# Optimization experiments

Measured on AMD Instinct MI355X. Metric: run time of the kernel, lower is better.

The kernel has to match this reference:

```python
import jax, jax.numpy as jnp
import numpy as np

H = W = 32      # latent grid
WS = 8          # window size
NH = 8          # heads
C = 512         # channels
SHIFTS = (0, WS // 2)  # depth-2 Swin stage: W-MSA then SW-MSA


def _rel_pos_index(ws):
    coords = np.stack(np.meshgrid(np.arange(ws), np.arange(ws), indexing='ij'))
    flat = coords.reshape(2, -1)
    rel = (flat[:, :, None] - flat[:, None, :]).transpose(1, 2, 0).copy()
    rel[:, :, 0] += ws - 1
    rel[:, :, 1] += ws - 1
    rel[:, :, 0] *= 2 * ws - 1
    return jnp.asarray(rel.sum(-1))  # (ws*ws, ws*ws) int


def _attn_mask(h, w, ws, shift):
    img = np.zeros((h, w))
    cnt = 0
    sl = (slice(0, -ws), slice(-ws, -shift), slice(-shift, None))
    for hs in sl:
        for wsl in sl:
            img[hs, wsl] = cnt
            cnt += 1
    mw = img.reshape(h // ws, ws, w // ws, ws).transpose(0, 2, 1, 3).reshape(-1, ws * ws)
    m = mw[:, None, :] - mw[:, :, None]  # matches unsqueeze(1) - unsqueeze(2)
    return jnp.asarray(np.where(m != 0, -100.0, 0.0).astype(np.float32))  # (nW, N, N)


def _ln(x, g, b, eps=1e-5):
    mu = x.mean(-1, keepdims=True)
    var = ((x - mu) ** 2).mean(-1, keepdims=True)
    return (x - mu) * jax.lax.rsqrt(var + eps) * g + b


def _swin_block(x, shift, mask, rpi, n1g, n1b, qw, qb, rpb, pw, pb, n2g, n2b, f1w, f1b, f2w, f2b):
    B, L, Cc = x.shape
    N = WS * WS
    hd = Cc // NH
    shortcut = x
    h = _ln(x, n1g, n1b).reshape(B, H, W, Cc)
    if shift > 0:
        h = jnp.roll(h, (-shift, -shift), (1, 2))
    # window partition -> (B*nW, N, C)
    hw = h.reshape(B, H // WS, WS, W // WS, WS, Cc).transpose(0, 1, 3, 2, 4, 5).reshape(-1, N, Cc)
    qkv = (hw @ qw + qb).reshape(-1, N, 3, NH, hd).transpose(2, 0, 3, 1, 4)
    q, k, v = qkv[0], qkv[1], qkv[2]
    attn = jnp.einsum('bhnd,bhmd->bhnm', q * (hd ** -0.5), k)
    bias = rpb[rpi.reshape(-1)].reshape(N, N, NH).transpose(2, 0, 1)  # (NH, N, N)
    attn = attn + bias[None]
    if mask is not None:
        nW = mask.shape[0]
        attn = attn.reshape(-1, nW, NH, N, N) + mask[None, :, None]
        attn = attn.reshape(-1, NH, N, N)
    attn = jax.nn.softmax(attn, axis=-1)
    o = jnp.einsum('bhnm,bhmd->bhnd', attn, v).transpose(0, 2, 1, 3).reshape(-1, N, Cc)
    o = o @ pw + pb
    # window reverse
    o = o.reshape(B, H // WS, W // WS, WS, WS, Cc).transpose(0, 1, 3, 2, 4, 5).reshape(B, H, W, Cc)
    if shift > 0:
        o = jnp.roll(o, (shift, shift), (1, 2))
    x = shortcut + o.reshape(B, L, Cc)
    h2 = _ln(x, n2g, n2b)
    x = x + (jax.nn.gelu(h2 @ f1w + f1b, approximate=False) @ f2w + f2b)
    return x


def setup_inputs() -> dict:
    key = jax.random.key(0)
    ks = jax.random.split(key, 8)
    B, D, K = 32, 2, 4096
    s = 0.02
    return {
        'x': jax.random.normal(ks[0], (B, H * W, C), jnp.float32),
        'norm1_g': jnp.ones((D, C), jnp.float32),
        'norm1_b': jnp.zeros((D, C), jnp.float32),
        'qkv_w': jax.random.normal(ks[1], (D, C, 3 * C), jnp.float32) * s,
        'qkv_b': jnp.zeros((D, 3 * C), jnp.float32),
        'rpb_table': jax.random.normal(ks[2], (D, (2 * WS - 1) ** 2, NH), jnp.float32) * s,
        'proj_w': jax.random.normal(ks[3], (D, C, C), jnp.float32) * s,
        'proj_b': jnp.zeros((D, C), jnp.float32),
        'norm2_g': jnp.ones((D, C), jnp.float32),
        'norm2_b': jnp.zeros((D, C), jnp.float32),
        'fc1_w': jax.random.normal(ks[4], (D, C, 4 * C), jnp.float32) * s,
        'fc1_b': jnp.zeros((D, 4 * C), jnp.float32),
        'fc2_w': jax.random.normal(ks[5], (D, 4 * C, C), jnp.float32) * s,
        'fc2_b': jnp.zeros((D, C), jnp.float32),
        'codebook': jax.random.normal(ks[6], (K, C), jnp.float32),
    }


def reference(x, norm1_g, norm1_b, qkv_w, qkv_b, rpb_table, proj_w, proj_b,
              norm2_g, norm2_b, fc1_w, fc1_b, fc2_w, fc2_b, codebook):
    B, L, Cc = x.shape
    rpi = _rel_pos_index(WS)
    masks = [None, _attn_mask(H, W, WS, SHIFTS[1])]
    for i, shift in enumerate(SHIFTS):
        x = _swin_block(x, shift, masks[i], rpi,
                        norm1_g[i], norm1_b[i], qkv_w[i], qkv_b[i], rpb_table[i],
                        proj_w[i], proj_b[i], norm2_g[i], norm2_b[i],
                        fc1_w[i], fc1_b[i], fc2_w[i], fc2_b[i])
    # nearest-neighbor codebook quantization (cdist + argmin + gather)
    flat = x.reshape(-1, Cc)
    d = ((flat ** 2).sum(-1, keepdims=True)
         - 2.0 * flat @ codebook.T
         + (codebook ** 2).sum(-1))  # (B*L, K)
    idx = jnp.argmin(d, axis=-1)
    quant = codebook[idx]
    # straight-through estimator
    quant = flat + jax.lax.stop_gradient(quant - flat)
    return quant.reshape(B, L, Cc), idx.reshape(B, L)
```

## Files before the change

### kernel.cpp

```cpp
#include <hip/hip_runtime.h>
#include <math.h>

#define DEV __device__ __forceinline__

typedef __attribute__((ext_vector_type(8))) _Float16 f16x8;
typedef __attribute__((ext_vector_type(8))) short short8;
typedef __attribute__((ext_vector_type(4))) float f32x4;

namespace {

constexpr int C = 512;
constexpr int ROWS = 32768;
constexpr float LSCALE = 2048.0f;
constexpr float LINV   = 1.0f / 2048.0f;
constexpr float F16MIN = 6.1035156e-5f;

DEV void f2hsplit(float x, short& hs, short& ls) {
  _Float16 h = (_Float16)x;
  float hf = (float)h;
  if (fabsf(hf) < F16MIN) { h = (_Float16)0.0f; hf = 0.f; }
  _Float16 l = (_Float16)((x - hf) * LSCALE);
  if (fabsf((float)l) < F16MIN) l = (_Float16)0.0f;
  hs = __builtin_bit_cast(short, h);
  ls = __builtin_bit_cast(short, l);
}

DEV unsigned umn(unsigned a, unsigned b) { return a < b ? a : b; }
DEV unsigned umx(unsigned a, unsigned b) { return a > b ? a : b; }

DEV unsigned packkey(float d, int col) {
  unsigned u = __builtin_bit_cast(unsigned, d);
  u = (u & 0x80000000u) ? ~u : (u | 0x80000000u);
  return (u & 0xFFFFF000u) | (unsigned)col;
}
DEV float unpackd(unsigned k) {
  unsigned u = (k & 0x80000000u) ? (k ^ 0x80000000u) : ~k;
  return __builtin_bit_cast(float, u);
}

DEV int rowmap(int r, int shift) {
  int b  = r >> 10;
  int w  = (r >> 6) & 15;
  int wy = w >> 2, wx = w & 3;
  int ii = r & 63;
  int iy = ii >> 3, ix = ii & 7;
  int y = (wy * 8 + iy + shift) & 31;
  int x = (wx * 8 + ix + shift) & 31;
  return (b << 10) + (y << 5) + x;
}

DEV int region(int y) { return (y < 24) ? 0 : ((y < 28) ? 1 : 2); }

typedef __attribute__((address_space(1))) const unsigned int gu32;
typedef __attribute__((address_space(3))) unsigned int lu32;
DEV void gload16(const void* g, void* l) {
  __builtin_amdgcn_global_load_lds((gu32*)g, (lu32*)l, 16, 0, 0);
}

DEV void tilemap(int Mt, int Nt, int GM, int& mt, int& nt) {
  int bid = blockIdx.y * Mt + blockIdx.x;
  if ((Mt & 7) == 0) {
    int xcd = bid & 7, idx = bid >> 3;
    int Mt8 = Mt >> 3;
    if (GM > Mt8) GM = Mt8;
    int span = GM * Nt;
    int g = idx / span, rem = idx % span;
    nt = rem / GM;
    mt = xcd * Mt8 + g * GM + rem % GM;
  } else {
    mt = blockIdx.x; nt = blockIdx.y;
  }
}

__global__ __launch_bounds__(256) void ln_split_kernel(
    const float* __restrict__ src, short* __restrict__ Hp, short* __restrict__ Lp,
    const float* __restrict__ g, const float* __restrict__ b,
    int shift, int windowed) {
  int wid  = (blockIdx.x * 256 + threadIdx.x) >> 6;
  int lane = threadIdx.x & 63;
  if (wid >= ROWS) return;
  int srcRow = windowed ? rowmap(wid, shift) : wid;
  const float* s = src + (size_t)srcRow * C + lane * 8;
  float v[8];
  *(float4*)(v)     = *(const float4*)(s);
  *(float4*)(v + 4) = *(const float4*)(s + 4);
  float sum = 0.f;
#pragma unroll
  for (int j = 0; j < 8; j++) sum += v[j];
#pragma unroll
  for (int o = 32; o >= 1; o >>= 1) sum += __shfl_xor(sum, o);
  float mu = sum * (1.0f / 512.0f);
  float vs = 0.f;
#pragma unroll
  for (int j = 0; j < 8; j++) { float d = v[j] - mu; vs += d * d; }
#pragma unroll
  for (int o = 32; o >= 1; o >>= 1) vs += __shfl_xor(vs, o);
  float rs = rsqrtf(vs * (1.0f / 512.0f) + 1e-5f);
  float gg[8], bb[8];
  *(float4*)gg       = *(const float4*)&g[lane * 8];
  *(float4*)(gg + 4) = *(const float4*)&g[lane * 8 + 4];
  *(float4*)bb       = *(const float4*)&b[lane * 8];
  *(float4*)(bb + 4) = *(const float4*)&b[lane * 8 + 4];
  short8 hv, lv;
#pragma unroll
  for (int j = 0; j < 8; j++) {
    float o8 = (v[j] - mu) * rs * gg[j] + bb[j];
    short hh, ll;
    f2hsplit(o8, hh, ll);
    hv[j] = hh; lv[j] = ll;
  }
  *(short8*)&Hp[(size_t)wid * C + lane * 8] = hv;
  *(short8*)&Lp[(size_t)wid * C + lane * 8] = lv;
}

__global__ __launch_bounds__(256) void rowss_kernel(
    const float* __restrict__ src, float* __restrict__ dst, int nrows) {
  int wid  = (blockIdx.x * 256 + threadIdx.x) >> 6;
  int lane = threadIdx.x & 63;
  if (wid >= nrows) return;
  const float* s = src + (size_t)wid * C + lane * 8;
  float4 a  = *(const float4*)s;
  float4 b4 = *(const float4*)(s + 4);
  float sum = a.x*a.x + a.y*a.y + a.z*a.z + a.w*a.w
            + b4.x*b4.x + b4.y*b4.y + b4.z*b4.z + b4.w*b4.w;
#pragma unroll
  for (int o = 32; o >= 1; o >>= 1) sum += __shfl_xor(sum, o);
  if (lane == 0) dst[wid] = sum;
}

__global__ __launch_bounds__(256) void wconvT_kernel(
    const float* __restrict__ W, short* __restrict__ Hp, short* __restrict__ Lp,
    int K, int N) {
  __shared__ float t[32][33];
  int tx = threadIdx.x, ty = threadIdx.y;
  int n0 = blockIdx.x * 32, k0 = blockIdx.y * 32;
#pragma unroll
  for (int r = 0; r < 4; r++) {
    int k = ty + r * 8;
    t[k][tx] = W[(size_t)(k0 + k) * N + n0 + tx];
  }
  __syncthreads();
#pragma unroll
  for (int r = 0; r < 4; r++) {
    int n = ty + r * 8;
    short h, l;
    f2hsplit(t[tx][n], h, l);
    Hp[(size_t)(n0 + n) * K + k0 + tx] = h;
    Lp[(size_t)(n0 + n) * K + k0 + tx] = l;
  }
}

__global__ __launch_bounds__(256) void wconv_kernel(
    const float* __restrict__ W, short* __restrict__ Hp, short* __restrict__ Lp) {
  size_t i = ((size_t)blockIdx.x * 256 + threadIdx.x) * 4;
  float4 a = *(const float4*)&W[i];
  float v[4] = {a.x, a.y, a.z, a.w};
  short hv[4], lv[4];
#pragma unroll
  for (int j = 0; j < 4; j++) f2hsplit(v[j], hv[j], lv[j]);
  *(short4*)&Hp[i] = *(short4*)hv;
  *(short4*)&Lp[i] = *(short4*)lv;
}

template <int EPI>
__global__ __launch_bounds__(512) void mgemm(
    const short* __restrict__ Ah, const short* __restrict__ Al,
    const short* __restrict__ Bh, const short* __restrict__ Bl,
    const int K, const float* __restrict__ bias,
    float* __restrict__ outF, short* __restrict__ outH, short* __restrict__ outL,
    const int ldo,
    const float* __restrict__ resid, const int rowOff, const int perm, const int shift) {
  __shared__ short lds[32768];
  int mt, nt;
  tilemap(gridDim.x, gridDim.y, 4, mt, nt);
  const int m0 = mt * 128, n0 = nt * 128;
  const int t  = threadIdx.x;
  const int wv = t >> 6, ln = t & 63;
  const int wr = (wv >> 2) * 64, wc = (wv & 3) * 32;
  const int l15 = ln & 15, l4 = ln >> 4;

  f32x4 accH[4][2], accL[4][2];
#pragma unroll
  for (int mf = 0; mf < 4; mf++)
#pragma unroll
    for (int nf = 0; nf < 2; nf++) {
      accH[mf][nf] = (f32x4){0.f, 0.f, 0.f, 0.f};
      accL[mf][nf] = (f32x4){0.f, 0.f, 0.f, 0.f};
    }

  const int srow = ln >> 2;
  const int scol = ((ln & 3) ^ ((ln >> 3) & 3)) * 8;

  auto stage = [&](int buf, int k0) {
    short* b = lds + buf * 16384;
    size_t ra = (size_t)(m0 + wv * 16 + srow) * K + k0 + scol;
    size_t rb = (size_t)(n0 + wv * 16 + srow) * K + k0 + scol;
    gload16(Ah + ra, b + wv * 512);
    gload16(Bh + rb, b + 4096 + wv * 512);
    gload16(Al + ra, b + 8192 + wv * 512);
    gload16(Bl + rb, b + 12288 + wv * 512);
  };
  auto frag = [&](const short* lt, int rbase) -> f16x8 {
    int r = rbase + l15;
    int kc = l4 ^ ((r >> 1) & 3);
    return *(const f16x8*)(lt + (r >> 4) * 512 + (r & 15) * 32 + kc * 8);
  };

  stage(0, 0);
  __syncthreads();
  int cur = 0;
  for (int k0 = 0; k0 < K; k0 += 32) {
    if (k0 + 32 < K) stage(cur ^ 1, k0 + 32);
    const short* base = lds + cur * 16384;
    f16x8 ah[4], bh[2], bl[2];
#pragma unroll
    for (int mf = 0; mf < 4; mf++) ah[mf] = frag(base, wr + mf * 16);
#pragma unroll
    for (int nf = 0; nf < 2; nf++) bh[nf] = frag(base + 4096, wc + nf * 16);
    __builtin_amdgcn_s_setprio(1);
#pragma unroll
    for (int mf = 0; mf < 4; mf++)
#pragma unroll
      for (int nf = 0; nf < 2; nf++)
        accH[mf][nf] = __builtin_amdgcn_mfma_f32_16x16x32_f16(ah[mf], bh[nf], accH[mf][nf], 0, 0, 0);
    __builtin_amdgcn_s_setprio(0);
#pragma unroll
    for (int nf = 0; nf < 2; nf++) bl[nf] = frag(base + 12288, wc + nf * 16);
    __builtin_amdgcn_s_setprio(1);
#pragma unroll
    for (int mf = 0; mf < 4; mf++)
#pragma unroll
      for (int nf = 0; nf < 2; nf++)
        accL[mf][nf] = __builtin_amdgcn_mfma_f32_16x16x32_f16(ah[mf], bl[nf], accL[mf][nf], 0, 0, 0);
#pragma unroll
    for (int mf = 0; mf < 4; mf++) {
      f16x8 al = frag(base + 8192, wr + mf * 16);
#pragma unroll
      for (int nf = 0; nf < 2; nf++)
        accL[mf][nf] = __builtin_amdgcn_mfma_f32_16x16x32_f16(al, bh[nf], accL[mf][nf], 0, 0, 0);
    }
    __builtin_amdgcn_s_setprio(0);
    __syncthreads();
    cur ^= 1;
  }

  f32x4 acc[4][2];
#pragma unroll
  for (int mf = 0; mf < 4; mf++)
#pragma unroll
    for (int nf = 0; nf < 2; nf++)
#pragma unroll
      for (int r = 0; r < 4; r++)
        acc[mf][nf][r] = fmaf(accL[mf][nf][r], LINV, accH[mf][nf][r]);

  if (EPI == 0) {
#pragma unroll
    for (int mf = 0; mf < 4; mf++)
#pragma unroll
      for (int r = 0; r < 4; r++) {
        int row = m0 + wr + mf * 16 + l4 * 4 + r;
        float* op = outF + (size_t)row * ldo;
#pragma unroll
        for (int nf = 0; nf < 2; nf++) {
          int col = n0 + wc + nf * 16 + l15;
          op[col] = acc[mf][nf][r] + bias[col];
        }
      }
  } else if (EPI == 1) {
#pragma unroll
    for (int mf = 0; mf < 4; mf++)
#pragma unroll
      for (int r = 0; r < 4; r++) {
        int row = m0 + wr + mf * 16 + l4 * 4 + r;
#pragma unroll
        for (int nf = 0; nf < 2; nf++) {
          int col = n0 + wc + nf * 16 + l15;
          float v = acc[mf][nf][r] + bias[col];
          v = 0.5f * v * (1.0f + erff(v * 0.70710678118654752f));
          short h, l;
          f2hsplit(v, h, l);
          outH[(size_t)row * ldo + col] = h;
          outL[(size_t)row * ldo + col] = l;
        }
      }
  } else {
#pragma unroll
    for (int mf = 0; mf < 4; mf++)
#pragma unroll
      for (int r = 0; r < 4; r++) {
        int row = m0 + wr + mf * 16 + l4 * 4 + r;
        int orow = perm ? rowmap(row, shift) : (row + rowOff);
        const float* rp = resid + (size_t)orow * ldo;
        float* op = outF + (size_t)orow * ldo;
#pragma unroll
        for (int nf = 0; nf < 2; nf++) {
          int col = n0 + wc + nf * 16 + l15;
          float v = rp[col] + acc[mf][nf][r] + bias[col];
          op[col] = v;
          if (EPI == 4) {
            short h, l;
            f2hsplit(v, h, l);
            outH[(size_t)orow * ldo + col] = h;
            outL[(size_t)orow * ldo + col] = l;
          }
        }
      }
  }
}

__global__ __launch_bounds__(512) void vqgemm(
    const short* __restrict__ Ah, const short* __restrict__ Bh,
    const float* __restrict__ c2, unsigned* __restrict__ pk) {
  __shared__ short lds[12288];
  const int bid = blockIdx.x;
  const int xcd = bid & 7, idx = bid >> 3;
  const int g  = idx >> 7;
  const int ny = (idx >> 3) & 15;
  const int mi = idx & 7;
  const int m0 = (xcd * 32 + g * 8 + mi) * 128;
  const int n0 = ny * 256;
  const int K = 512;
  const int t  = threadIdx.x;
  const int wv = t >> 6, ln = t & 63;
  const int wr = (wv >> 2) * 64, wc = (wv & 3) * 64;
  const int l15 = ln & 15, l4 = ln >> 4;

  f32x4 acc[4][4];
#pragma unroll
  for (int mf = 0; mf < 4; mf++)
#pragma unroll
    for (int nf = 0; nf < 4; nf++) acc[mf][nf] = (f32x4){0.f, 0.f, 0.f, 0.f};

  const int srow = ln >> 2;
  const int scol = ((ln & 3) ^ ((ln >> 3) & 3)) * 8;

  short* As = lds;
  short* Bs = lds + 4096;

  auto frag = [&](const short* lt, int rbase) -> f16x8 {
    int r = rbase + l15;
    int kc = l4 ^ ((r >> 1) & 3);
    return *(const f16x8*)(lt + (r >> 4) * 512 + (r & 15) * 32 + kc * 8);
  };

  for (int k0 = 0; k0 < K; k0 += 32) {
#pragma unroll
    for (int q = 0; q < 3; q++) {
      int s = wv * 3 + q;
      int isA = (s < 8);
      int c = isA ? s : (s - 8);
      const short* src = isA ? Ah : Bh;
      short* dst = (isA ? As : Bs) + c * 512;
      int rowbase = (isA ? m0 : n0) + c * 16;
      size_t ga = (size_t)(rowbase + srow) * K + k0 + scol;
      gload16(src + ga, dst);
    }
    __syncthreads();
    f16x8 ah[4], bh[4];
#pragma unroll
    for (int mf = 0; mf < 4; mf++) ah[mf] = frag(As, wr + mf * 16);
#pragma unroll
    for (int nf = 0; nf < 4; nf++) bh[nf] = frag(Bs, wc + nf * 16);
    __builtin_amdgcn_s_setprio(1);
#pragma unroll
    for (int mf = 0; mf < 4; mf++)
#pragma unroll
      for (int nf = 0; nf < 4; nf++)
        acc[mf][nf] = __builtin_amdgcn_mfma_f32_16x16x32_f16(ah[mf], bh[nf], acc[mf][nf], 0, 0, 0);
    __builtin_amdgcn_s_setprio(0);
    __syncthreads();
  }

  unsigned* hk = (unsigned*)(void*)lds;
#pragma unroll
  for (int mf = 0; mf < 4; mf++)
#pragma unroll
    for (int r = 0; r < 4; r++) {
      int wrow = wr + mf * 16 + l4 * 4 + r;
      unsigned k1 = 0xFFFFFFFFu, k2 = 0xFFFFFFFFu;
#pragma unroll
      for (int nf = 0; nf < 4; nf++) {
        int col = n0 + wc + nf * 16 + l15;
        float d = c2[col] - 2.0f * acc[mf][nf][r];
        unsigned kk = packkey(d, col);
        if (kk < k1) { k2 = k1; k1 = kk; }
        else if (kk < k2) { k2 = kk; }
      }
#pragma unroll
      for (int o = 1; o <= 8; o <<= 1) {
        unsigned b1 = (unsigned)__shfl_xor((int)k1, o);
        unsigned b2 = (unsigned)__shfl_xor((int)k2, o);
        unsigned m1 = umn(k1, b1);
        unsigned m2 = umn(umx(k1, b1), umn(k2, b2));
        k1 = m1; k2 = m2;
      }
      if (l15 == 0) {
        hk[wrow * 8 + (wv & 3) * 2 + 0] = k1;
        hk[wrow * 8 + (wv & 3) * 2 + 1] = k2;
      }
    }
  __syncthreads();
  if (t < 128) {
    unsigned q1[4], q2[4];
#pragma unroll
    for (int i = 0; i < 4; i++) {
      q1[i] = hk[t * 8 + i * 2];
      q2[i] = hk[t * 8 + i * 2 + 1];
    }
    unsigned a1 = umn(q1[0], q1[1]);
    unsigned a2 = umn(umx(q1[0], q1[1]), umn(q2[0], q2[1]));
    unsigned b1 = umn(q1[2], q1[3]);
    unsigned b2 = umn(umx(q1[2], q1[3]), umn(q2[2], q2[3]));
    unsigned m1 = umn(a1, b1);
    unsigned m2 = umn(umx(a1, b1), umn(a2, b2));
    size_t base = (size_t)(m0 + t) * 32 + ny * 2;
    pk[base + 0] = m1;
    pk[base + 1] = m2;
  }
}

__global__ __launch_bounds__(256) void vq_out_kernel(
    const unsigned* __restrict__ pk, const float* __restrict__ x,
    const float* __restrict__ cb,
    float* __restrict__ outq, float* __restrict__ outidx) {
  int r = blockIdx.x * 4 + (threadIdx.x >> 6);
  int lane = threadIdx.x & 63;
  unsigned key = (lane < 32) ? pk[(size_t)r * 32 + lane] : 0xFFFFFFFFu;
  unsigned kmin = key;
#pragma unroll
  for (int o = 32; o >= 1; o >>= 1) kmin = umn(kmin, (unsigned)__shfl_xor((int)kmin, o));
  float dmin = unpackd(kmin);
  unsigned long long mask = __ballot(lane < 32 && unpackd(key) <= dmin + 2.0f);

  const float* xr = x + (size_t)r * C + lane * 8;
  float4 xa = *(const float4*)xr;
  float4 xb = *(const float4*)(xr + 4);

  float bestd = 3.4e38f;
  int   besti = 0x7fffffff;
  while (mask) {
    int l = __ffsll(mask) - 1;
    mask &= mask - 1;
    int col = ((unsigned)__shfl((int)key, l)) & 0xFFFu;
    const float* cr = cb + (size_t)col * C + lane * 8;
    float4 ca = *(const float4*)cr;
    float4 cb4 = *(const float4*)(cr + 4);
    float s = 0.f;
    s = fmaf(ca.x, ca.x - 2.f * xa.x, s);
    s = fmaf(ca.y, ca.y - 2.f * xa.y, s);
    s = fmaf(ca.z, ca.z - 2.f * xa.z, s);
    s = fmaf(ca.w, ca.w - 2.f * xa.w, s);
    s = fmaf(cb4.x, cb4.x - 2.f * xb.x, s);
    s = fmaf(cb4.y, cb4.y - 2.f * xb.y, s);
    s = fmaf(cb4.z, cb4.z - 2.f * xb.z, s);
    s = fmaf(cb4.w, cb4.w - 2.f * xb.w, s);
#pragma unroll
    for (int o = 32; o >= 1; o >>= 1) s += __shfl_xor(s, o);
    if (s < bestd || (s == bestd && col < besti)) { bestd = s; besti = col; }
  }
  const float4* src = (const float4*)(cb + (size_t)besti * C + lane * 8);
  float4*       dst = (float4*)(outq + (size_t)r * C + lane * 8);
  dst[0] = src[0];
  dst[1] = src[1];
  if (lane == 0) outidx[r] = (float)besti;
}

__global__ __launch_bounds__(256) void attn_kernel(
    const float* __restrict__ qkv,
    const float* __restrict__ rpb,
    short* __restrict__ Hout, short* __restrict__ Lout,
    int winOff, int shift) {
  int wl = blockIdx.x;
  int h  = blockIdx.y;
  int t  = threadIdx.x;
  __shared__ float q[64][64], k[64][64], v[64][64];
  float (*pT)[64] = q;

  const float* base = qkv + (size_t)wl * 64 * 1536 + h * 64;
#pragma unroll
  for (int rep = 0; rep < 4; rep++) {
    int f = t + rep * 256;
    int i = f >> 4, dq = (f & 15) * 4;
    const float* rowp = base + (size_t)i * 1536 + dq;
    float4 qv = *(const float4*)(rowp);
    float4 kv = *(const float4*)(rowp + 512);
    float4 vv = *(const float4*)(rowp + 1024);
    q[i][dq] = qv.x * 0.125f; q[i][dq + 1] = qv.y * 0.125f;
    q[i][dq + 2] = qv.z * 0.125f; q[i][dq + 3] = qv.w * 0.125f;
    *(float4*)&k[i][dq] = kv;
    *(float4*)&v[i][dq] = vv;
  }
  __syncthreads();

  int i  = t >> 2;
  int jg = t & 3;
  int wim = (winOff + wl) & 15;
  int wy = wim >> 2, wx = wim & 3;
  int iy = i >> 3, ix = i & 7;

  float qreg[64];
#pragma unroll
  for (int d = 0; d < 64; d += 4) *(float4*)&qreg[d] = *(float4*)&q[i][d];
  __syncthreads();

  int ci = 0;
  if (shift) ci = region(wy * 8 + iy) * 3 + region(wx * 8 + ix);

  float sc[16];
#pragma unroll
  for (int jj = 0; jj < 16; jj++) {
    int j = jg * 16 + jj;
    float s = 0.f;
#pragma unroll
    for (int d = 0; d < 64; d += 4) {
      float4 kv = *(float4*)&k[j][d];
      s = fmaf(qreg[d], kv.x, s);
      s = fmaf(qreg[d + 1], kv.y, s);
      s = fmaf(qreg[d + 2], kv.z, s);
      s = fmaf(qreg[d + 3], kv.w, s);
    }
    int jy = j >> 3, jx = j & 7;
    s += rpb[((iy - jy + 7) * 15 + (ix - jx + 7)) * 8 + h];
    if (shift) {
      int cj = region(wy * 8 + jy) * 3 + region(wx * 8 + jx);
      if (ci != cj) s -= 100.0f;
    }
    sc[jj] = s;
  }
  float mx = sc[0];
#pragma unroll
  for (int jj = 1; jj < 16; jj++) mx = fmaxf(mx, sc[jj]);
  mx = fmaxf(mx, __shfl_xor(mx, 1));
  mx = fmaxf(mx, __shfl_xor(mx, 2));
  float sum = 0.f;
#pragma unroll
  for (int jj = 0; jj < 16; jj++) { sc[jj] = expf(sc[jj] - mx); sum += sc[jj]; }
  sum += __shfl_xor(sum, 1);
  sum += __shfl_xor(sum, 2);
  float inv = 1.0f / sum;
#pragma unroll
  for (int jj = 0; jj < 16; jj++) pT[jg * 16 + jj][i] = sc[jj] * inv;
  __syncthreads();

  float accv[16];
#pragma unroll
  for (int dd = 0; dd < 16; dd++) accv[dd] = 0.f;
  for (int j = 0; j < 64; j++) {
    float pij = pT[j][i];
#pragma unroll
    for (int dd = 0; dd < 16; dd += 4) {
      float4 vv = *(float4*)&v[j][jg * 16 + dd];
      accv[dd]     = fmaf(pij, vv.x, accv[dd]);
      accv[dd + 1] = fmaf(pij, vv.y, accv[dd + 1]);
      accv[dd + 2] = fmaf(pij, vv.z, accv[dd + 2]);
      accv[dd + 3] = fmaf(pij, vv.w, accv[dd + 3]);
    }
  }
  size_t obase = ((size_t)(winOff + wl) * 64 + i) * 512 + h * 64 + jg * 16;
  short8 hv, lv;
#pragma unroll
  for (int half = 0; half < 2; half++) {
#pragma unroll
    for (int j = 0; j < 8; j++) {
      short hh, ll;
      f2hsplit(accv[half * 8 + j], hh, ll);
      hv[j] = hh; lv[j] = ll;
    }
    *(short8*)&Hout[obase + half * 8] = hv;
    *(short8*)&Lout[obase + half * 8] = lv;
  }
}

}

extern "C" void kernel_launch(void* const* d_in, const int* in_sizes, int n_in,
                              void* d_out, int out_size, void* d_ws, size_t ws_size,
                              hipStream_t stream) {
  const float* x_in = (const float*)d_in[0];
  const float* n1g  = (const float*)d_in[1];
  const float* n1b  = (const float*)d_in[2];
  const float* qkvw = (const float*)d_in[3];
  const float* qkvb = (const float*)d_in[4];
  const float* rpb  = (const float*)d_in[5];
  const float* pw   = (const float*)d_in[6];
  const float* pb   = (const float*)d_in[7];
  const float* n2g  = (const float*)d_in[8];
  const float* n2b  = (const float*)d_in[9];
  const float* f1w  = (const float*)d_in[10];
  const float* f1b  = (const float*)d_in[11];
  const float* f2w  = (const float*)d_in[12];
  const float* f2b_ = (const float*)d_in[13];
  const float* cb   = (const float*)d_in[14];

  float* outq   = (float*)d_out;
  float* outidx = outq + 16777216;
  short* Hbuf = (short*)d_out;
  short* Lbuf = Hbuf + (size_t)ROWS * 512;

  char* ws = (char*)d_ws;
  float* Abuf = (float*)ws;
  short* Wb   = (short*)(ws + ((size_t)64 << 20));
  char*  Cbuf = ws + ((size_t)96 << 20);
  const int Rrows = (ws_size >= ((size_t)232 << 20)) ? 16384
                  : (ws_size >= ((size_t)160 << 20)) ? 8192
                  : (ws_size >= ((size_t)128 << 20)) ? 4096 : 2048;

  const int SZ_QKV = 512 * 1536, SZ_P = 512 * 512, SZ_F1 = 512 * 2048, SZ_F2 = 2048 * 512;
  const int PB = (SZ_QKV + SZ_P + SZ_F1 + SZ_F2) * 2;
  short* cbH = Wb + (size_t)2 * PB;
  short* cbL = cbH + 4096 * 512;

  for (int blk = 0; blk < 2; blk++) {
    short* base = Wb + (size_t)blk * PB;
    short* qH = base;          short* qL = qH + SZ_QKV;
    short* pH = qL + SZ_QKV;   short* pL = pH + SZ_P;
    short* f1H = pL + SZ_P;    short* f1L = f1H + SZ_F1;
    short* f2H = f1L + SZ_F1;  short* f2L = f2H + SZ_F2;
    wconvT_kernel<<<dim3(48, 16), dim3(32, 8), 0, stream>>>(qkvw + (size_t)blk * SZ_QKV, qH, qL, 512, 1536);
    wconvT_kernel<<<dim3(16, 16), dim3(32, 8), 0, stream>>>(pw + (size_t)blk * SZ_P, pH, pL, 512, 512);
    wconvT_kernel<<<dim3(64, 16), dim3(32, 8), 0, stream>>>(f1w + (size_t)blk * SZ_F1, f1H, f1L, 512, 2048);
    wconvT_kernel<<<dim3(16, 64), dim3(32, 8), 0, stream>>>(f2w + (size_t)blk * SZ_F2, f2H, f2L, 2048, 512);
  }
  wconv_kernel<<<2048, 256, 0, stream>>>(cb, cbH, cbL);

  const int nch = ROWS / Rrows;
  for (int blk = 0; blk < 2; blk++) {
    short* base = Wb + (size_t)blk * PB;
    short* qH = base;          short* qL = qH + SZ_QKV;
    short* pH = qL + SZ_QKV;   short* pL = pH + SZ_P;
    short* f1H = pL + SZ_P;    short* f1L = f1H + SZ_F1;
    short* f2H = f1L + SZ_F1;  short* f2L = f2H + SZ_F2;
    const float* xcur = blk ? (const float*)Abuf : x_in;
    int shift = blk ? 4 : 0;

    ln_split_kernel<<<8192, 256, 0, stream>>>(xcur, Hbuf, Lbuf, n1g + blk * 512, n1b + blk * 512, shift, 1);

    float* Cq = (float*)Cbuf;
    for (int ch = 0; ch < nch; ch++) {
      int r0 = ch * Rrows;
      mgemm<0><<<dim3(Rrows / 128, 12), 512, 0, stream>>>(
          Hbuf + (size_t)r0 * 512, Lbuf + (size_t)r0 * 512, qH, qL, 512,
          qkvb + blk * 1536, Cq, nullptr, nullptr, 1536,
          nullptr, 0, 0, 0);
      attn_kernel<<<dim3(Rrows / 64, 8), 256, 0, stream>>>(
          Cq, rpb + blk * 1800, Hbuf, Lbuf, r0 >> 6, shift);
    }

    mgemm<2><<<dim3(256, 4), 512, 0, stream>>>(
        Hbuf, Lbuf, pH, pL, 512, pb + blk * 512,
        Abuf, nullptr, nullptr, 512,
        blk ? (const float*)Abuf : x_in, 0, 1, shift);

    ln_split_kernel<<<8192, 256, 0, stream>>>(Abuf, Hbuf, Lbuf, n2g + blk * 512, n2b + blk * 512, 0, 0);

    short* gh = (short*)Cbuf;
    short* gl = gh + (size_t)Rrows * 2048;
    for (int ch = 0; ch < nch; ch++) {
      int r0 = ch * Rrows;
      mgemm<1><<<dim3(Rrows / 128, 16), 512, 0, stream>>>(
          Hbuf + (size_t)r0 * 512, Lbuf + (size_t)r0 * 512, f1H, f1L, 512,
          f1b + blk * 2048, nullptr, gh, gl, 2048,
          nullptr, 0, 0, 0);
      if (blk == 0) {
        mgemm<2><<<dim3(Rrows / 128, 4), 512, 0, stream>>>(
            gh, gl, f2H, f2L, 2048, f2b_ + blk * 512,
            Abuf, nullptr, nullptr, 512,
            Abuf, r0, 0, 0);
      } else {
        mgemm<4><<<dim3(Rrows / 128, 4), 512, 0, stream>>>(
            gh, gl, f2H, f2L, 2048, f2b_ + blk * 512,
            Abuf, Hbuf, Lbuf, 512,
            Abuf, r0, 0, 0);
      }
    }
  }

  float*    c2  = (float*)Cbuf;
  unsigned* pkb = (unsigned*)(Cbuf + ((size_t)64 << 10));
  rowss_kernel<<<1024, 256, 0, stream>>>(cb, c2, 4096);
  vqgemm<<<4096, 512, 0, stream>>>(Hbuf, cbH, c2, pkb);
  vq_out_kernel<<<8192, 256, 0, stream>>>(pkb, Abuf, cb, outq, outidx);
}
```

Before: 2.237 ms.

## Retile attention kernel into 4x4 register blocks with padded shared memory

```diff
diff --git a/kernel.cpp b/kernel.cpp
--- a/kernel.cpp
+++ b/kernel.cpp
@@ -470,11 +470,13 @@
     const float* __restrict__ rpb,
     short* __restrict__ Hout, short* __restrict__ Lout,
     int winOff, int shift) {
+  constexpr int LDW = 68;
+  __shared__ float q[64 * LDW], k[64 * LDW], v[64 * LDW];
+  float* pT = q;
+
   int wl = blockIdx.x;
   int h  = blockIdx.y;
   int t  = threadIdx.x;
-  __shared__ float q[64][64], k[64][64], v[64][64];
-  float (*pT)[64] = q;
 
   const float* base = qkv + (size_t)wl * 64 * 1536 + h * 64;
 #pragma unroll
@@ -485,89 +487,116 @@
     float4 qv = *(const float4*)(rowp);
     float4 kv = *(const float4*)(rowp + 512);
     float4 vv = *(const float4*)(rowp + 1024);
-    q[i][dq] = qv.x * 0.125f; q[i][dq + 1] = qv.y * 0.125f;
-    q[i][dq + 2] = qv.z * 0.125f; q[i][dq + 3] = qv.w * 0.125f;
-    *(float4*)&k[i][dq] = kv;
-    *(float4*)&v[i][dq] = vv;
+    qv.x *= 0.125f; qv.y *= 0.125f; qv.z *= 0.125f; qv.w *= 0.125f;
+    *(float4*)&q[i * LDW + dq] = qv;
+    *(float4*)&k[i * LDW + dq] = kv;
+    *(float4*)&v[i * LDW + dq] = vv;
   }
   __syncthreads();
 
-  int i  = t >> 2;
-  int jg = t & 3;
-  int wim = (winOff + wl) & 15;
-  int wy = wim >> 2, wx = wim & 3;
-  int iy = i >> 3, ix = i & 7;
-
-  float qreg[64];
-#pragma unroll
-  for (int d = 0; d < 64; d += 4) *(float4*)&qreg[d] = *(float4*)&q[i][d];
+  const int rgrp = t >> 4, cgrp = t & 15;
+  const int wim = (winOff + wl) & 15;
+  const int wy = wim >> 2, wx = wim & 3;
+
+  float s[4][4];
+#pragma unroll
+  for (int r = 0; r < 4; r++)
+#pragma unroll
+    for (int c = 0; c < 4; c++) s[r][c] = 0.f;
+#pragma unroll
+  for (int dch = 0; dch < 16; dch++) {
+    float4 q4[4], k4[4];
+#pragma unroll
+    for (int r = 0; r < 4; r++) q4[r] = *(float4*)&q[(rgrp * 4 + r) * LDW + dch * 4];
+#pragma unroll
+    for (int c = 0; c < 4; c++) k4[c] = *(float4*)&k[(cgrp + 16 * c) * LDW + dch * 4];
+#pragma unroll
+    for (int r = 0; r < 4; r++)
+#pragma unroll
+      for (int c = 0; c < 4; c++) {
+        s[r][c] = fmaf(q4[r].x, k4[c].x, s[r][c]);
+        s[r][c] = fmaf(q4[r].y, k4[c].y, s[r][c]);
+        s[r][c] = fmaf(q4[r].z, k4[c].z, s[r][c]);
+        s[r][c] = fmaf(q4[r].w, k4[c].w, s[r][c]);
+      }
+  }
+#pragma unroll
+  for (int r = 0; r < 4; r++) {
+    int i = rgrp * 4 + r;
+    int iy = i >> 3, ix = i & 7;
+    int ci = shift ? (region(wy * 8 + iy) * 3 + region(wx * 8 + ix)) : 0;
+#pragma unroll
+    for (int c = 0; c < 4; c++) {
+      int j = cgrp + 16 * c;
+      int jy = j >> 3, jx = j & 7;
+      s[r][c] += rpb[((iy - jy + 7) * 15 + (ix - jx + 7)) * 8 + h];
+      if (shift) {
+        int cj = region(wy * 8 + jy) * 3 + region(wx * 8 + jx);
+        if (ci != cj) s[r][c] -= 100.0f;
+      }
+    }
+  }
+  float p[4][4];
+#pragma unroll
+  for (int r = 0; r < 4; r++) {
+    float mx = fmaxf(fmaxf(s[r][0], s[r][1]), fmaxf(s[r][2], s[r][3]));
+#pragma unroll
+    for (int o = 1; o <= 8; o <<= 1) mx = fmaxf(mx, __shfl_xor(mx, o));
+    float sum = 0.f;
+#pragma unroll
+    for (int c = 0; c < 4; c++) { p[r][c] = expf(s[r][c] - mx); sum += p[r][c]; }
+#pragma unroll
+    for (int o = 1; o <= 8; o <<= 1) sum += __shfl_xor(sum, o);
+    float inv = 1.0f / sum;
+#pragma unroll
+    for (int c = 0; c < 4; c++) p[r][c] *= inv;
+  }
   __syncthreads();
-
-  int ci = 0;
-  if (shift) ci = region(wy * 8 + iy) * 3 + region(wx * 8 + ix);
-
-  float sc[16];
-#pragma unroll
-  for (int jj = 0; jj < 16; jj++) {
-    int j = jg * 16 + jj;
-    float s = 0.f;
-#pragma unroll
-    for (int d = 0; d < 64; d += 4) {
-      float4 kv = *(float4*)&k[j][d];
-      s = fmaf(qreg[d], kv.x, s);
-      s = fmaf(qreg[d + 1], kv.y, s);
-      s = fmaf(qreg[d + 2], kv.z, s);
-      s = fmaf(qreg[d + 3], kv.w, s);
-    }
-    int jy = j >> 3, jx = j & 7;
-    s += rpb[((iy - jy + 7) * 15 + (ix - jx + 7)) * 8 + h];
-    if (shift) {
-      int cj = region(wy * 8 + jy) * 3 + region(wx * 8 + jx);
-      if (ci != cj) s -= 100.0f;
-    }
-    sc[jj] = s;
-  }
-  float mx = sc[0];
-#pragma unroll
-  for (int jj = 1; jj < 16; jj++) mx = fmaxf(mx, sc[jj]);
-  mx = fmaxf(mx, __shfl_xor(mx, 1));
-  mx = fmaxf(mx, __shfl_xor(mx, 2));
-  float sum = 0.f;
-#pragma unroll
-  for (int jj = 0; jj < 16; jj++) { sc[jj] = expf(sc[jj] - mx); sum += sc[jj]; }
-  sum += __shfl_xor(sum, 1);
-  sum += __shfl_xor(sum, 2);
-  float inv = 1.0f / sum;
-#pragma unroll
-  for (int jj = 0; jj < 16; jj++) pT[jg * 16 + jj][i] = sc[jj] * inv;
+#pragma unroll
+  for (int c = 0; c < 4; c++) {
+    int j = cgrp + 16 * c;
+    float4 pw;
+    pw.x = p[0][c]; pw.y = p[1][c]; pw.z = p[2][c]; pw.w = p[3][c];
+    *(float4*)&pT[j * LDW + rgrp * 4] = pw;
+  }
   __syncthreads();
 
-  float accv[16];
-#pragma unroll
-  for (int dd = 0; dd < 16; dd++) accv[dd] = 0.f;
+  float o4[4][4];
+#pragma unroll
+  for (int r = 0; r < 4; r++)
+#pragma unroll
+    for (int e = 0; e < 4; e++) o4[r][e] = 0.f;
+#pragma unroll 8
   for (int j = 0; j < 64; j++) {
-    float pij = pT[j][i];
-#pragma unroll
-    for (int dd = 0; dd < 16; dd += 4) {
-      float4 vv = *(float4*)&v[j][jg * 16 + dd];
-      accv[dd]     = fmaf(pij, vv.x, accv[dd]);
-      accv[dd + 1] = fmaf(pij, vv.y, accv[dd + 1]);
-      accv[dd + 2] = fmaf(pij, vv.z, accv[dd + 2]);
-      accv[dd + 3] = fmaf(pij, vv.w, accv[dd + 3]);
-    }
-  }
-  size_t obase = ((size_t)(winOff + wl) * 64 + i) * 512 + h * 64 + jg * 16;
-  short8 hv, lv;
-#pragma unroll
-  for (int half = 0; half < 2; half++) {
-#pragma unroll
-    for (int j = 0; j < 8; j++) {
-      short hh, ll;
-      f2hsplit(accv[half * 8 + j], hh, ll);
-      hv[j] = hh; lv[j] = ll;
-    }
-    *(short8*)&Hout[obase + half * 8] = hv;
-    *(short8*)&Lout[obase + half * 8] = lv;
+    float4 pv4 = *(float4*)&pT[j * LDW + rgrp * 4];
+    float4 vv4 = *(float4*)&v[j * LDW + cgrp * 4];
+    o4[0][0] = fmaf(pv4.x, vv4.x, o4[0][0]);
+    o4[0][1] = fmaf(pv4.x, vv4.y, o4[0][1]);
+    o4[0][2] = fmaf(pv4.x, vv4.z, o4[0][2]);
+    o4[0][3] = fmaf(pv4.x, vv4.w, o4[0][3]);
+    o4[1][0] = fmaf(pv4.y, vv4.x, o4[1][0]);
+    o4[1][1] = fmaf(pv4.y, vv4.y, o4[1][1]);
+    o4[1][2] = fmaf(pv4.y, vv4.z, o4[1][2]);
+    o4[1][3] = fmaf(pv4.y, vv4.w, o4[1][3]);
+    o4[2][0] = fmaf(pv4.z, vv4.x, o4[2][0]);
+    o4[2][1] = fmaf(pv4.z, vv4.y, o4[2][1]);
+    o4[2][2] = fmaf(pv4.z, vv4.z, o4[2][2]);
+    o4[2][3] = fmaf(pv4.z, vv4.w, o4[2][3]);
+    o4[3][0] = fmaf(pv4.w, vv4.x, o4[3][0]);
+    o4[3][1] = fmaf(pv4.w, vv4.y, o4[3][1]);
+    o4[3][2] = fmaf(pv4.w, vv4.z, o4[3][2]);
+    o4[3][3] = fmaf(pv4.w, vv4.w, o4[3][3]);
+  }
+  size_t rowbase = (size_t)(winOff + wl) * 64;
+#pragma unroll
+  for (int r = 0; r < 4; r++) {
+    int i = rgrp * 4 + r;
+    size_t ob = (rowbase + i) * 512 + h * 64 + cgrp * 4;
+    short hv4[4], lv4[4];
+#pragma unroll
+    for (int e = 0; e < 4; e++) f2hsplit(o4[r][e], hv4[e], lv4[e]);
+    *(short4*)&Hout[ob] = *(short4*)hv4;
+    *(short4*)&Lout[ob] = *(short4*)lv4;
   }
 }
 
```

Result: faster. 2.068 ms (-7.6%).
